# Optimization experiments

Measured on AMD Instinct MI355X. Metric: run time of the kernel, lower is better.

## Reference

```python
import jax, jax.numpy as jnp
import numpy as np

N = 50000
E = 800000
F_IN = 128
F_OUT = 128


def setup_inputs() -> dict:
    key = jax.random.key(0)
    ks = jax.random.split(key, 7)
    feature = jax.random.normal(ks[0], (N, F_IN), dtype=jnp.float32)
    self_weight = jax.random.uniform(ks[1], (N, 1), dtype=jnp.float32)
    weight = jax.random.uniform(ks[2], (E,), dtype=jnp.float32)
    src = jax.random.randint(ks[3], (E,), 0, N, dtype=jnp.int32)
    dst = jax.random.randint(ks[4], (E,), 0, N, dtype=jnp.int32)
    W = jax.random.normal(ks[5], (F_OUT, F_IN), dtype=jnp.float32) / np.sqrt(F_IN)
    b = jax.random.normal(ks[6], (F_OUT,), dtype=jnp.float32) * 0.01
    return {"feature": feature, "self_weight": self_weight, "weight": weight,
            "src": src, "dst": dst, "W": W, "b": b}


def reference(feature, self_weight, weight, src, dst, W, b):
    # messages: (w + 1) * h_src  -> [E, F_IN]
    msgs = (weight + 1.0)[:, None] * feature[src]
    # segment-sum into destination nodes -> [N, F_IN]
    agg = jax.ops.segment_sum(msgs, dst, num_segments=N)
    # self-loop affine: h * (self_weight + 1) + aggregated messages
    h = feature * (self_weight + 1.0) + agg
    # final linear: h @ W^T + b
    return h @ W.T + b
```

## Files before the change

kernel.cpp:

```cpp
#include <hip/hip_runtime.h>


#define F 128
#define NPB 32
#define CAPB 1408
#define CHUNK 4096
#define MAXNB 1600

typedef __attribute__((ext_vector_type(8))) short short8;
typedef __attribute__((ext_vector_type(4))) float f32x4;

__device__ inline unsigned short f2b(float f) {
    union { float f; unsigned u; } v; v.f = f;
    unsigned r = (v.u + 0x7fffu + ((v.u >> 16) & 1u)) >> 16;
    return (unsigned short)r;
}
__device__ inline float blo(unsigned u) { union { unsigned u; float f; } x; x.u = u << 16; return x.f; }
__device__ inline float bhi(unsigned u) { union { unsigned u; float f; } x; x.u = u & 0xffff0000u; return x.f; }

struct __align__(8) Edge { unsigned pk; float w; };

__global__ __launch_bounds__(256) void gemm_scatter(
    const float* __restrict__ feat, const float* __restrict__ W,
    const int* __restrict__ dst, const int* __restrict__ src,
    const float* __restrict__ weight,
    unsigned short* __restrict__ g, int* __restrict__ gcur,
    Edge* __restrict__ sorted, int M, int E, int GB, int NB)
{
    __shared__ __align__(16) char smem[128 * 136 * 2 + 64 * 136 * 2];
    const int tid = threadIdx.x;

    if ((int)blockIdx.x < GB) {
        unsigned short* Wl  = (unsigned short*)smem;
        unsigned short* ftl = (unsigned short*)(smem + 128 * 136 * 2);
        const int row0 = blockIdx.x * 64;

        for (int i = tid; i < 128 * 32; i += 256) {
            int r = i >> 5, c4 = i & 31;
            float4 v = ((const float4*)W)[i];
            ushort4 h; h.x = f2b(v.x); h.y = f2b(v.y); h.z = f2b(v.z); h.w = f2b(v.w);
            *(ushort4*)&Wl[r * 136 + c4 * 4] = h;
        }
        for (int i = tid; i < 64 * 32; i += 256) {
            int r = i >> 5, c4 = i & 31;
            int rr = row0 + r; if (rr >= M) rr = M - 1;
            float4 v = ((const float4*)feat)[(size_t)rr * 32 + c4];
            ushort4 h; h.x = f2b(v.x); h.y = f2b(v.y); h.z = f2b(v.z); h.w = f2b(v.w);
            *(ushort4*)&ftl[r * 136 + c4 * 4] = h;
        }
        __syncthreads();

        const int lane = tid & 63, wid = tid >> 6;
        const int m = lane & 15, quad = lane >> 4;
        const int rbase = wid * 16;

        f32x4 acc[8];
#pragma unroll
        for (int t = 0; t < 8; ++t) acc[t] = (f32x4){0.f, 0.f, 0.f, 0.f};

#pragma unroll
        for (int kk = 0; kk < 4; ++kk) {
            const int k0 = kk * 32 + quad * 8;
            short8 a = *(const short8*)&ftl[(rbase + m) * 136 + k0];
#pragma unroll
            for (int t = 0; t < 8; ++t) {
                short8 bfrag = *(const short8*)&Wl[(t * 16 + m) * 136 + k0];
                acc[t] = __builtin_amdgcn_mfma_f32_16x16x32_bf16(a, bfrag, acc[t], 0, 0, 0);
            }
        }

#pragma unroll
        for (int reg = 0; reg < 4; ++reg) {
            int r = row0 + rbase + quad * 4 + reg;
            if (r < M) {
#pragma unroll
                for (int t = 0; t < 8; ++t)
                    g[(size_t)r * F + t * 16 + m] = f2b(acc[t][reg]);
            }
        }
    } else {
        int* hist  = (int*)smem;
        int* lbase = hist + MAXNB;
        const int e0 = ((int)blockIdx.x - GB) * CHUNK;

        for (int i = tid; i < NB; i += 256) hist[i] = 0;
        __syncthreads();
#pragma unroll
        for (int j = 0; j < CHUNK / 256; ++j) {
            int e = e0 + j * 256 + tid;
            if (e < E) atomicAdd(&hist[dst[e] >> 5], 1);
        }
        __syncthreads();
        for (int i = tid; i < NB; i += 256) {
            int c = hist[i];
            lbase[i] = c ? atomicAdd(&gcur[i], c) : 0;
            hist[i] = 0;
        }
        __syncthreads();
#pragma unroll
        for (int j = 0; j < CHUNK / 256; ++j) {
            int e = e0 + j * 256 + tid;
            if (e < E) {
                int d = dst[e];
                int bkt = d >> 5;
                int pos = lbase[bkt] + atomicAdd(&hist[bkt], 1);
                if (pos < CAPB) {
                    Edge ed;
                    ed.pk = (unsigned)src[e] | ((unsigned)(d & 31) << 16);
                    ed.w = weight[e] + 1.0f;
                    sorted[(size_t)bkt * CAPB + pos] = ed;
                }
            }
        }
    }
}

__global__ __launch_bounds__(256, 6) void bucket_gather(
    const unsigned short* __restrict__ g, const Edge* __restrict__ sorted,
    const int* __restrict__ gcur, const float* __restrict__ sw,
    const float* __restrict__ bvec, float* __restrict__ out, int M)
{
    __shared__ Edge ebuf[CAPB];
    __shared__ int hcnt[NPB];
    __shared__ int off[NPB + 1];
    __shared__ int cur[NPB];

    const int b = blockIdx.x, tid = threadIdx.x;
    int cnt = gcur[b]; if (cnt > CAPB) cnt = CAPB;

    if (tid < NPB) hcnt[tid] = 0;
    __syncthreads();

    Edge held[(CAPB + 255) / 256];
    int nh = 0;
    for (int i = tid; i < cnt; i += 256) {
        Edge e = sorted[(size_t)b * CAPB + i];
        held[nh++] = e;
        atomicAdd(&hcnt[e.pk >> 16], 1);
    }
    __syncthreads();
    if (tid < NPB) {
        int v = hcnt[tid];
        int x = v;
#pragma unroll
        for (int s = 1; s < NPB; s <<= 1) {
            int t = __shfl_up(x, s, 64);
            if (tid >= s) x += t;
        }
        off[tid + 1] = x;
        if (tid == 0) off[0] = 0;
        cur[tid] = x - v;
    }
    __syncthreads();
    for (int j = 0; j < nh; ++j) {
        int dl = held[j].pk >> 16;
        int p = atomicAdd(&cur[dl], 1);
        ebuf[p] = held[j];
    }
    __syncthreads();

    const int grp = tid >> 4, c = tid & 15;
    const float4 b0 = ((const float4*)bvec)[c * 2];
    const float4 b1 = ((const float4*)bvec)[c * 2 + 1];

    for (int nn = grp; nn < NPB; nn += 16) {
        const int node = b * NPB + nn;
        if (node >= M) continue;
        int p = off[nn];
        const int pe = off[nn + 1];

        float acc[8] = {0.f, 0.f, 0.f, 0.f, 0.f, 0.f, 0.f, 0.f};
        for (; p + 1 < pe; p += 2) {
            Edge e0 = ebuf[p], e1 = ebuf[p + 1];
            const uint4 r0 = *(const uint4*)(g + (size_t)(e0.pk & 0xffffu) * F + c * 8);
            const uint4 r1 = *(const uint4*)(g + (size_t)(e1.pk & 0xffffu) * F + c * 8);
            float w0 = e0.w, w1 = e1.w;
            acc[0] = fmaf(w0, blo(r0.x), acc[0]); acc[1] = fmaf(w0, bhi(r0.x), acc[1]);
            acc[2] = fmaf(w0, blo(r0.y), acc[2]); acc[3] = fmaf(w0, bhi(r0.y), acc[3]);
            acc[4] = fmaf(w0, blo(r0.z), acc[4]); acc[5] = fmaf(w0, bhi(r0.z), acc[5]);
            acc[6] = fmaf(w0, blo(r0.w), acc[6]); acc[7] = fmaf(w0, bhi(r0.w), acc[7]);
            acc[0] = fmaf(w1, blo(r1.x), acc[0]); acc[1] = fmaf(w1, bhi(r1.x), acc[1]);
            acc[2] = fmaf(w1, blo(r1.y), acc[2]); acc[3] = fmaf(w1, bhi(r1.y), acc[3]);
            acc[4] = fmaf(w1, blo(r1.z), acc[4]); acc[5] = fmaf(w1, bhi(r1.z), acc[5]);
            acc[6] = fmaf(w1, blo(r1.w), acc[6]); acc[7] = fmaf(w1, bhi(r1.w), acc[7]);
        }
        if (p < pe) {
            Edge e0 = ebuf[p];
            const uint4 r0 = *(const uint4*)(g + (size_t)(e0.pk & 0xffffu) * F + c * 8);
            float w0 = e0.w;
            acc[0] = fmaf(w0, blo(r0.x), acc[0]); acc[1] = fmaf(w0, bhi(r0.x), acc[1]);
            acc[2] = fmaf(w0, blo(r0.y), acc[2]); acc[3] = fmaf(w0, bhi(r0.y), acc[3]);
            acc[4] = fmaf(w0, blo(r0.z), acc[4]); acc[5] = fmaf(w0, bhi(r0.z), acc[5]);
            acc[6] = fmaf(w0, blo(r0.w), acc[6]); acc[7] = fmaf(w0, bhi(r0.w), acc[7]);
        }

        const uint4 sr = *(const uint4*)(g + (size_t)node * F + c * 8);
        const float s = sw[node] + 1.0f;
        float4 o0, o1;
        o0.x = fmaf(s, blo(sr.x), b0.x) + acc[0];
        o0.y = fmaf(s, bhi(sr.x), b0.y) + acc[1];
        o0.z = fmaf(s, blo(sr.y), b0.z) + acc[2];
        o0.w = fmaf(s, bhi(sr.y), b0.w) + acc[3];
        o1.x = fmaf(s, blo(sr.z), b1.x) + acc[4];
        o1.y = fmaf(s, bhi(sr.z), b1.y) + acc[5];
        o1.z = fmaf(s, blo(sr.w), b1.z) + acc[6];
        o1.w = fmaf(s, bhi(sr.w), b1.w) + acc[7];
        float4* o = (float4*)(out + (size_t)node * F + c * 8);
        o[0] = o0; o[1] = o1;
    }
}

extern "C" void kernel_launch(void* const* d_in, const int* in_sizes, int n_in,
                              void* d_out, int out_size, void* d_ws, size_t ws_size,
                              hipStream_t stream) {
    const float* feat   = (const float*)d_in[0];
    const float* sw     = (const float*)d_in[1];
    const float* weight = (const float*)d_in[2];
    const int*   src    = (const int*)  d_in[3];
    const int*   dst    = (const int*)  d_in[4];
    const float* W      = (const float*)d_in[5];
    const float* b      = (const float*)d_in[6];
    float* out = (float*)d_out;

    const int M = in_sizes[1];
    const int E = in_sizes[2];
    const int NB = (M + NPB - 1) / NPB;
    const int GB = (M + 63) / 64;
    const int SB = (E + CHUNK - 1) / CHUNK;

    char* ws = (char*)d_ws;
    size_t og    = 0;
    size_t ocur  = ((og   + (size_t)M * F * 2) + 255) & ~(size_t)255;
    size_t osort = ((ocur + (size_t)NB * 4) + 255) & ~(size_t)255;

    unsigned short* g = (unsigned short*)(ws + og);
    int*  gcur   = (int*)(ws + ocur);
    Edge* sorted = (Edge*)(ws + osort);

    hipMemsetAsync(gcur, 0, (size_t)NB * 4, stream);
    gemm_scatter<<<GB + SB, 256, 0, stream>>>(
        feat, W, dst, src, weight, g, gcur, sorted, M, E, GB, NB);
    bucket_gather<<<NB, 256, 0, stream>>>(g, sorted, gcur, sw, b, out, M);
}
```

Measured before the change: 158.4 us.

## Split gather buckets across two blocks and read W fragments directly from global

The gather kernel now launches two blocks per 32-node bucket, each handling 16 destination nodes. Each block rescans the bucket's edge list twice from global memory instead of holding edges in registers, which doubles the parallelism and removes the per-node loop. The GEMM blocks no longer stage W into shared memory; each lane loads its W fragment from global (expected to hit cache) and converts it to bf16 inline. The aim is to cut LDS footprint and register pressure to raise occupancy, at the cost of redundant edge reads and repeated W conversions.

```diff
diff --git a/kernel.cpp b/kernel.cpp
--- a/kernel.cpp
+++ b/kernel.cpp
@@ -4,6 +4,7 @@
 #define F 128
 #define NPB 32
 #define CAPB 1408
+#define CAPH 896
 #define CHUNK 4096
 #define MAXNB 1600
 
@@ -27,20 +28,13 @@
     unsigned short* __restrict__ g, int* __restrict__ gcur,
     Edge* __restrict__ sorted, int M, int E, int GB, int NB)
 {
-    __shared__ __align__(16) char smem[128 * 136 * 2 + 64 * 136 * 2];
+    __shared__ __align__(16) char smem[64 * 136 * 2];
     const int tid = threadIdx.x;
 
     if ((int)blockIdx.x < GB) {
-        unsigned short* Wl  = (unsigned short*)smem;
-        unsigned short* ftl = (unsigned short*)(smem + 128 * 136 * 2);
+        unsigned short* ftl = (unsigned short*)smem;
         const int row0 = blockIdx.x * 64;
 
-        for (int i = tid; i < 128 * 32; i += 256) {
-            int r = i >> 5, c4 = i & 31;
-            float4 v = ((const float4*)W)[i];
-            ushort4 h; h.x = f2b(v.x); h.y = f2b(v.y); h.z = f2b(v.z); h.w = f2b(v.w);
-            *(ushort4*)&Wl[r * 136 + c4 * 4] = h;
-        }
         for (int i = tid; i < 64 * 32; i += 256) {
             int r = i >> 5, c4 = i & 31;
             int rr = row0 + r; if (rr >= M) rr = M - 1;
@@ -64,8 +58,14 @@
             short8 a = *(const short8*)&ftl[(rbase + m) * 136 + k0];
 #pragma unroll
             for (int t = 0; t < 8; ++t) {
-                short8 bfrag = *(const short8*)&Wl[(t * 16 + m) * 136 + k0];
-                acc[t] = __builtin_amdgcn_mfma_f32_16x16x32_bf16(a, bfrag, acc[t], 0, 0, 0);
+                const float4 w0 = *(const float4*)&W[(size_t)(t * 16 + m) * F + k0];
+                const float4 w1 = *(const float4*)&W[(size_t)(t * 16 + m) * F + k0 + 4];
+                short8 bf;
+                bf[0] = (short)f2b(w0.x); bf[1] = (short)f2b(w0.y);
+                bf[2] = (short)f2b(w0.z); bf[3] = (short)f2b(w0.w);
+                bf[4] = (short)f2b(w1.x); bf[5] = (short)f2b(w1.y);
+                bf[6] = (short)f2b(w1.z); bf[7] = (short)f2b(w1.w);
+                acc[t] = __builtin_amdgcn_mfma_f32_16x16x32_bf16(a, bf, acc[t], 0, 0, 0);
             }
         }
 
@@ -115,35 +115,34 @@
     }
 }
 
-__global__ __launch_bounds__(256, 6) void bucket_gather(
+__global__ __launch_bounds__(256) void bucket_gather(
     const unsigned short* __restrict__ g, const Edge* __restrict__ sorted,
     const int* __restrict__ gcur, const float* __restrict__ sw,
     const float* __restrict__ bvec, float* __restrict__ out, int M)
 {
-    __shared__ Edge ebuf[CAPB];
-    __shared__ int hcnt[NPB];
-    __shared__ int off[NPB + 1];
-    __shared__ int cur[NPB];
-
-    const int b = blockIdx.x, tid = threadIdx.x;
+    __shared__ Edge ebuf[CAPH];
+    __shared__ int hcnt[16];
+    __shared__ int off[17];
+    __shared__ int cur[16];
+
+    const int tid = threadIdx.x;
+    const int b = blockIdx.x >> 1, half = blockIdx.x & 1;
     int cnt = gcur[b]; if (cnt > CAPB) cnt = CAPB;
-
-    if (tid < NPB) hcnt[tid] = 0;
-    __syncthreads();
-
-    Edge held[(CAPB + 255) / 256];
-    int nh = 0;
+    const Edge* sb = sorted + (size_t)b * CAPB;
+
+    if (tid < 16) hcnt[tid] = 0;
+    __syncthreads();
+
     for (int i = tid; i < cnt; i += 256) {
-        Edge e = sorted[(size_t)b * CAPB + i];
-        held[nh++] = e;
-        atomicAdd(&hcnt[e.pk >> 16], 1);
-    }
-    __syncthreads();
-    if (tid < NPB) {
+        int dl = sb[i].pk >> 16;
+        if ((dl >> 4) == half) atomicAdd(&hcnt[dl & 15], 1);
+    }
+    __syncthreads();
+    if (tid < 16) {
         int v = hcnt[tid];
         int x = v;
 #pragma unroll
-        for (int s = 1; s < NPB; s <<= 1) {
+        for (int s = 1; s < 16; s <<= 1) {
             int t = __shfl_up(x, s, 64);
             if (tid >= s) x += t;
         }
@@ -152,62 +151,63 @@
         cur[tid] = x - v;
     }
     __syncthreads();
-    for (int j = 0; j < nh; ++j) {
-        int dl = held[j].pk >> 16;
-        int p = atomicAdd(&cur[dl], 1);
-        ebuf[p] = held[j];
+    for (int i = tid; i < cnt; i += 256) {
+        Edge e = sb[i];
+        int dl = e.pk >> 16;
+        if ((dl >> 4) == half) {
+            int p = atomicAdd(&cur[dl & 15], 1);
+            if (p < CAPH) ebuf[p] = e;
+        }
     }
     __syncthreads();
 
     const int grp = tid >> 4, c = tid & 15;
+    const int node = b * NPB + half * 16 + grp;
+    if (node >= M) return;
+    int p = off[grp];
+    int pe = off[grp + 1]; if (pe > CAPH) pe = CAPH;
+
     const float4 b0 = ((const float4*)bvec)[c * 2];
     const float4 b1 = ((const float4*)bvec)[c * 2 + 1];
 
-    for (int nn = grp; nn < NPB; nn += 16) {
-        const int node = b * NPB + nn;
-        if (node >= M) continue;
-        int p = off[nn];
-        const int pe = off[nn + 1];
-
-        float acc[8] = {0.f, 0.f, 0.f, 0.f, 0.f, 0.f, 0.f, 0.f};
-        for (; p + 1 < pe; p += 2) {
-            Edge e0 = ebuf[p], e1 = ebuf[p + 1];
-            const uint4 r0 = *(const uint4*)(g + (size_t)(e0.pk & 0xffffu) * F + c * 8);
-            const uint4 r1 = *(const uint4*)(g + (size_t)(e1.pk & 0xffffu) * F + c * 8);
-            float w0 = e0.w, w1 = e1.w;
-            acc[0] = fmaf(w0, blo(r0.x), acc[0]); acc[1] = fmaf(w0, bhi(r0.x), acc[1]);
-            acc[2] = fmaf(w0, blo(r0.y), acc[2]); acc[3] = fmaf(w0, bhi(r0.y), acc[3]);
-            acc[4] = fmaf(w0, blo(r0.z), acc[4]); acc[5] = fmaf(w0, bhi(r0.z), acc[5]);
-            acc[6] = fmaf(w0, blo(r0.w), acc[6]); acc[7] = fmaf(w0, bhi(r0.w), acc[7]);
-            acc[0] = fmaf(w1, blo(r1.x), acc[0]); acc[1] = fmaf(w1, bhi(r1.x), acc[1]);
-            acc[2] = fmaf(w1, blo(r1.y), acc[2]); acc[3] = fmaf(w1, bhi(r1.y), acc[3]);
-            acc[4] = fmaf(w1, blo(r1.z), acc[4]); acc[5] = fmaf(w1, bhi(r1.z), acc[5]);
-            acc[6] = fmaf(w1, blo(r1.w), acc[6]); acc[7] = fmaf(w1, bhi(r1.w), acc[7]);
-        }
-        if (p < pe) {
-            Edge e0 = ebuf[p];
-            const uint4 r0 = *(const uint4*)(g + (size_t)(e0.pk & 0xffffu) * F + c * 8);
-            float w0 = e0.w;
-            acc[0] = fmaf(w0, blo(r0.x), acc[0]); acc[1] = fmaf(w0, bhi(r0.x), acc[1]);
-            acc[2] = fmaf(w0, blo(r0.y), acc[2]); acc[3] = fmaf(w0, bhi(r0.y), acc[3]);
-            acc[4] = fmaf(w0, blo(r0.z), acc[4]); acc[5] = fmaf(w0, bhi(r0.z), acc[5]);
-            acc[6] = fmaf(w0, blo(r0.w), acc[6]); acc[7] = fmaf(w0, bhi(r0.w), acc[7]);
-        }
-
-        const uint4 sr = *(const uint4*)(g + (size_t)node * F + c * 8);
-        const float s = sw[node] + 1.0f;
-        float4 o0, o1;
-        o0.x = fmaf(s, blo(sr.x), b0.x) + acc[0];
-        o0.y = fmaf(s, bhi(sr.x), b0.y) + acc[1];
-        o0.z = fmaf(s, blo(sr.y), b0.z) + acc[2];
-        o0.w = fmaf(s, bhi(sr.y), b0.w) + acc[3];
-        o1.x = fmaf(s, blo(sr.z), b1.x) + acc[4];
-        o1.y = fmaf(s, bhi(sr.z), b1.y) + acc[5];
-        o1.z = fmaf(s, blo(sr.w), b1.z) + acc[6];
-        o1.w = fmaf(s, bhi(sr.w), b1.w) + acc[7];
-        float4* o = (float4*)(out + (size_t)node * F + c * 8);
-        o[0] = o0; o[1] = o1;
-    }
+    float acc[8] = {0.f, 0.f, 0.f, 0.f, 0.f, 0.f, 0.f, 0.f};
+    for (; p + 1 < pe; p += 2) {
+        Edge e0 = ebuf[p], e1 = ebuf[p + 1];
+        const uint4 r0 = *(const uint4*)(g + (size_t)(e0.pk & 0xffffu) * F + c * 8);
+        const uint4 r1 = *(const uint4*)(g + (size_t)(e1.pk & 0xffffu) * F + c * 8);
+        float w0 = e0.w, w1 = e1.w;
+        acc[0] = fmaf(w0, blo(r0.x), acc[0]); acc[1] = fmaf(w0, bhi(r0.x), acc[1]);
+        acc[2] = fmaf(w0, blo(r0.y), acc[2]); acc[3] = fmaf(w0, bhi(r0.y), acc[3]);
+        acc[4] = fmaf(w0, blo(r0.z), acc[4]); acc[5] = fmaf(w0, bhi(r0.z), acc[5]);
+        acc[6] = fmaf(w0, blo(r0.w), acc[6]); acc[7] = fmaf(w0, bhi(r0.w), acc[7]);
+        acc[0] = fmaf(w1, blo(r1.x), acc[0]); acc[1] = fmaf(w1, bhi(r1.x), acc[1]);
+        acc[2] = fmaf(w1, blo(r1.y), acc[2]); acc[3] = fmaf(w1, bhi(r1.y), acc[3]);
+        acc[4] = fmaf(w1, blo(r1.z), acc[4]); acc[5] = fmaf(w1, bhi(r1.z), acc[5]);
+        acc[6] = fmaf(w1, blo(r1.w), acc[6]); acc[7] = fmaf(w1, bhi(r1.w), acc[7]);
+    }
+    if (p < pe) {
+        Edge e0 = ebuf[p];
+        const uint4 r0 = *(const uint4*)(g + (size_t)(e0.pk & 0xffffu) * F + c * 8);
+        float w0 = e0.w;
+        acc[0] = fmaf(w0, blo(r0.x), acc[0]); acc[1] = fmaf(w0, bhi(r0.x), acc[1]);
+        acc[2] = fmaf(w0, blo(r0.y), acc[2]); acc[3] = fmaf(w0, bhi(r0.y), acc[3]);
+        acc[4] = fmaf(w0, blo(r0.z), acc[4]); acc[5] = fmaf(w0, bhi(r0.z), acc[5]);
+        acc[6] = fmaf(w0, blo(r0.w), acc[6]); acc[7] = fmaf(w0, bhi(r0.w), acc[7]);
+    }
+
+    const uint4 sr = *(const uint4*)(g + (size_t)node * F + c * 8);
+    const float s = sw[node] + 1.0f;
+    float4 o0, o1;
+    o0.x = fmaf(s, blo(sr.x), b0.x) + acc[0];
+    o0.y = fmaf(s, bhi(sr.x), b0.y) + acc[1];
+    o0.z = fmaf(s, blo(sr.y), b0.z) + acc[2];
+    o0.w = fmaf(s, bhi(sr.y), b0.w) + acc[3];
+    o1.x = fmaf(s, blo(sr.z), b1.x) + acc[4];
+    o1.y = fmaf(s, bhi(sr.z), b1.y) + acc[5];
+    o1.z = fmaf(s, blo(sr.w), b1.z) + acc[6];
+    o1.w = fmaf(s, bhi(sr.w), b1.w) + acc[7];
+    float4* o = (float4*)(out + (size_t)node * F + c * 8);
+    o[0] = o0; o[1] = o1;
 }
 
 extern "C" void kernel_launch(void* const* d_in, const int* in_sizes, int n_in,
@@ -240,5 +240,5 @@
     hipMemsetAsync(gcur, 0, (size_t)NB * 4, stream);
     gemm_scatter<<<GB + SB, 256, 0, stream>>>(
         feat, W, dst, src, weight, g, gcur, sorted, M, E, GB, NB);
-    bucket_gather<<<NB, 256, 0, stream>>>(g, sorted, gcur, sw, b, out, M);
-}
+    bucket_gather<<<NB * 2, 256, 0, stream>>>(g, sorted, gcur, sw, b, out, M);
+}
```

Measured after the change: 161.4 us. No clear change (+1.9%).

## Split bucket gather across column slices and load GEMM A operand directly

Applied to the files above, without the earlier changes.

Bucket size doubles to 64 nodes with larger edge chunks and capacity. The gather kernel now launches eight blocks per bucket, each covering a 16-column slice, and each block re-sorts the bucket's edges in shared memory. That trades redundant edge sorting for more parallelism and smaller per-thread loads. The GEMM path drops the shared-memory staging of feature rows and converts them to bf16 straight from global loads into MFMA fragments. Scatter blocks are moved ahead of GEMM blocks in the grid order.

```diff
diff --git a/kernel.cpp b/kernel.cpp
--- a/kernel.cpp
+++ b/kernel.cpp
@@ -2,10 +2,10 @@
 
 
 #define F 128
-#define NPB 32
-#define CAPB 1408
-#define CHUNK 4096
-#define MAXNB 1600
+#define NPB 64
+#define CAPB 2560
+#define CHUNK 16384
+#define MAXNB 800
 
 typedef __attribute__((ext_vector_type(8))) short short8;
 typedef __attribute__((ext_vector_type(4))) float f32x4;
@@ -25,34 +25,28 @@
     const int* __restrict__ dst, const int* __restrict__ src,
     const float* __restrict__ weight,
     unsigned short* __restrict__ g, int* __restrict__ gcur,
-    Edge* __restrict__ sorted, int M, int E, int GB, int NB)
+    Edge* __restrict__ sorted, int M, int E, int SB, int NB)
 {
-    __shared__ __align__(16) char smem[128 * 136 * 2 + 64 * 136 * 2];
+    __shared__ __align__(16) char smem[128 * 136 * 2];
     const int tid = threadIdx.x;
 
-    if ((int)blockIdx.x < GB) {
-        unsigned short* Wl  = (unsigned short*)smem;
-        unsigned short* ftl = (unsigned short*)(smem + 128 * 136 * 2);
-        const int row0 = blockIdx.x * 64;
-
-        for (int i = tid; i < 128 * 32; i += 256) {
+    if ((int)blockIdx.x >= SB) {
+        unsigned short* Wl = (unsigned short*)smem;
+        const int row0 = ((int)blockIdx.x - SB) * 64;
+
+        for (int i = tid; i < 4096; i += 256) {
             int r = i >> 5, c4 = i & 31;
             float4 v = ((const float4*)W)[i];
             ushort4 h; h.x = f2b(v.x); h.y = f2b(v.y); h.z = f2b(v.z); h.w = f2b(v.w);
             *(ushort4*)&Wl[r * 136 + c4 * 4] = h;
         }
-        for (int i = tid; i < 64 * 32; i += 256) {
-            int r = i >> 5, c4 = i & 31;
-            int rr = row0 + r; if (rr >= M) rr = M - 1;
-            float4 v = ((const float4*)feat)[(size_t)rr * 32 + c4];
-            ushort4 h; h.x = f2b(v.x); h.y = f2b(v.y); h.z = f2b(v.z); h.w = f2b(v.w);
-            *(ushort4*)&ftl[r * 136 + c4 * 4] = h;
-        }
         __syncthreads();
 
         const int lane = tid & 63, wid = tid >> 6;
         const int m = lane & 15, quad = lane >> 4;
         const int rbase = wid * 16;
+        int rr = row0 + rbase + m; if (rr >= M) rr = M - 1;
+        const float* frow = feat + (size_t)rr * F;
 
         f32x4 acc[8];
 #pragma unroll
@@ -61,7 +55,13 @@
 #pragma unroll
         for (int kk = 0; kk < 4; ++kk) {
             const int k0 = kk * 32 + quad * 8;
-            short8 a = *(const short8*)&ftl[(rbase + m) * 136 + k0];
+            const float4 a0 = *(const float4*)&frow[k0];
+            const float4 a1 = *(const float4*)&frow[k0 + 4];
+            short8 a;
+            a[0] = (short)f2b(a0.x); a[1] = (short)f2b(a0.y);
+            a[2] = (short)f2b(a0.z); a[3] = (short)f2b(a0.w);
+            a[4] = (short)f2b(a1.x); a[5] = (short)f2b(a1.y);
+            a[6] = (short)f2b(a1.z); a[7] = (short)f2b(a1.w);
 #pragma unroll
             for (int t = 0; t < 8; ++t) {
                 short8 bfrag = *(const short8*)&Wl[(t * 16 + m) * 136 + k0];
@@ -81,14 +81,13 @@
     } else {
         int* hist  = (int*)smem;
         int* lbase = hist + MAXNB;
-        const int e0 = ((int)blockIdx.x - GB) * CHUNK;
+        const int e0 = (int)blockIdx.x * CHUNK;
 
         for (int i = tid; i < NB; i += 256) hist[i] = 0;
         __syncthreads();
-#pragma unroll
         for (int j = 0; j < CHUNK / 256; ++j) {
             int e = e0 + j * 256 + tid;
-            if (e < E) atomicAdd(&hist[dst[e] >> 5], 1);
+            if (e < E) atomicAdd(&hist[dst[e] >> 6], 1);
         }
         __syncthreads();
         for (int i = tid; i < NB; i += 256) {
@@ -97,16 +96,15 @@
             hist[i] = 0;
         }
         __syncthreads();
-#pragma unroll
         for (int j = 0; j < CHUNK / 256; ++j) {
             int e = e0 + j * 256 + tid;
             if (e < E) {
                 int d = dst[e];
-                int bkt = d >> 5;
+                int bkt = d >> 6;
                 int pos = lbase[bkt] + atomicAdd(&hist[bkt], 1);
                 if (pos < CAPB) {
                     Edge ed;
-                    ed.pk = (unsigned)src[e] | ((unsigned)(d & 31) << 16);
+                    ed.pk = (unsigned)src[e] | ((unsigned)(d & 63) << 16);
                     ed.w = weight[e] + 1.0f;
                     sorted[(size_t)bkt * CAPB + pos] = ed;
                 }
@@ -115,7 +113,7 @@
     }
 }
 
-__global__ __launch_bounds__(256, 6) void bucket_gather(
+__global__ __launch_bounds__(256) void bucket_gather(
     const unsigned short* __restrict__ g, const Edge* __restrict__ sorted,
     const int* __restrict__ gcur, const float* __restrict__ sw,
     const float* __restrict__ bvec, float* __restrict__ out, int M)
@@ -125,89 +123,72 @@
     __shared__ int off[NPB + 1];
     __shared__ int cur[NPB];
 
-    const int b = blockIdx.x, tid = threadIdx.x;
+    const int tid = threadIdx.x;
+    const int s = (int)blockIdx.x & 7;
+    const int b = (int)blockIdx.x >> 3;
     int cnt = gcur[b]; if (cnt > CAPB) cnt = CAPB;
+    const Edge* sb = sorted + (size_t)b * CAPB;
 
     if (tid < NPB) hcnt[tid] = 0;
     __syncthreads();
-
-    Edge held[(CAPB + 255) / 256];
-    int nh = 0;
-    for (int i = tid; i < cnt; i += 256) {
-        Edge e = sorted[(size_t)b * CAPB + i];
-        held[nh++] = e;
-        atomicAdd(&hcnt[e.pk >> 16], 1);
-    }
+    for (int i = tid; i < cnt; i += 256)
+        atomicAdd(&hcnt[sb[i].pk >> 16], 1);
     __syncthreads();
     if (tid < NPB) {
         int v = hcnt[tid];
         int x = v;
 #pragma unroll
-        for (int s = 1; s < NPB; s <<= 1) {
-            int t = __shfl_up(x, s, 64);
-            if (tid >= s) x += t;
+        for (int st = 1; st < NPB; st <<= 1) {
+            int t = __shfl_up(x, st, 64);
+            if (tid >= st) x += t;
         }
         off[tid + 1] = x;
         if (tid == 0) off[0] = 0;
         cur[tid] = x - v;
     }
     __syncthreads();
-    for (int j = 0; j < nh; ++j) {
-        int dl = held[j].pk >> 16;
-        int p = atomicAdd(&cur[dl], 1);
-        ebuf[p] = held[j];
-    }
-    __syncthreads();
-
-    const int grp = tid >> 4, c = tid & 15;
-    const float4 b0 = ((const float4*)bvec)[c * 2];
-    const float4 b1 = ((const float4*)bvec)[c * 2 + 1];
-
-    for (int nn = grp; nn < NPB; nn += 16) {
-        const int node = b * NPB + nn;
-        if (node >= M) continue;
-        int p = off[nn];
-        const int pe = off[nn + 1];
-
-        float acc[8] = {0.f, 0.f, 0.f, 0.f, 0.f, 0.f, 0.f, 0.f};
-        for (; p + 1 < pe; p += 2) {
-            Edge e0 = ebuf[p], e1 = ebuf[p + 1];
-            const uint4 r0 = *(const uint4*)(g + (size_t)(e0.pk & 0xffffu) * F + c * 8);
-            const uint4 r1 = *(const uint4*)(g + (size_t)(e1.pk & 0xffffu) * F + c * 8);
-            float w0 = e0.w, w1 = e1.w;
-            acc[0] = fmaf(w0, blo(r0.x), acc[0]); acc[1] = fmaf(w0, bhi(r0.x), acc[1]);
-            acc[2] = fmaf(w0, blo(r0.y), acc[2]); acc[3] = fmaf(w0, bhi(r0.y), acc[3]);
-            acc[4] = fmaf(w0, blo(r0.z), acc[4]); acc[5] = fmaf(w0, bhi(r0.z), acc[5]);
-            acc[6] = fmaf(w0, blo(r0.w), acc[6]); acc[7] = fmaf(w0, bhi(r0.w), acc[7]);
-            acc[0] = fmaf(w1, blo(r1.x), acc[0]); acc[1] = fmaf(w1, bhi(r1.x), acc[1]);
-            acc[2] = fmaf(w1, blo(r1.y), acc[2]); acc[3] = fmaf(w1, bhi(r1.y), acc[3]);
-            acc[4] = fmaf(w1, blo(r1.z), acc[4]); acc[5] = fmaf(w1, bhi(r1.z), acc[5]);
-            acc[6] = fmaf(w1, blo(r1.w), acc[6]); acc[7] = fmaf(w1, bhi(r1.w), acc[7]);
-        }
-        if (p < pe) {
-            Edge e0 = ebuf[p];
-            const uint4 r0 = *(const uint4*)(g + (size_t)(e0.pk & 0xffffu) * F + c * 8);
-            float w0 = e0.w;
-            acc[0] = fmaf(w0, blo(r0.x), acc[0]); acc[1] = fmaf(w0, bhi(r0.x), acc[1]);
-            acc[2] = fmaf(w0, blo(r0.y), acc[2]); acc[3] = fmaf(w0, bhi(r0.y), acc[3]);
-            acc[4] = fmaf(w0, blo(r0.z), acc[4]); acc[5] = fmaf(w0, bhi(r0.z), acc[5]);
-            acc[6] = fmaf(w0, blo(r0.w), acc[6]); acc[7] = fmaf(w0, bhi(r0.w), acc[7]);
-        }
-
-        const uint4 sr = *(const uint4*)(g + (size_t)node * F + c * 8);
-        const float s = sw[node] + 1.0f;
-        float4 o0, o1;
-        o0.x = fmaf(s, blo(sr.x), b0.x) + acc[0];
-        o0.y = fmaf(s, bhi(sr.x), b0.y) + acc[1];
-        o0.z = fmaf(s, blo(sr.y), b0.z) + acc[2];
-        o0.w = fmaf(s, bhi(sr.y), b0.w) + acc[3];
-        o1.x = fmaf(s, blo(sr.z), b1.x) + acc[4];
-        o1.y = fmaf(s, bhi(sr.z), b1.y) + acc[5];
-        o1.z = fmaf(s, blo(sr.w), b1.z) + acc[6];
-        o1.w = fmaf(s, bhi(sr.w), b1.w) + acc[7];
-        float4* o = (float4*)(out + (size_t)node * F + c * 8);
-        o[0] = o0; o[1] = o1;
-    }
+    for (int i = tid; i < cnt; i += 256) {
+        Edge e = sb[i];
+        int p = atomicAdd(&cur[e.pk >> 16], 1);
+        ebuf[p] = e;
+    }
+    __syncthreads();
+
+    const int grp = tid >> 2, l = tid & 3;
+    const int node = b * NPB + grp;
+    if (node >= M) return;
+    const int cb = s * 16 + l * 4;
+    int p = off[grp];
+    const int pe = off[grp + 1];
+
+    float acc[4] = {0.f, 0.f, 0.f, 0.f};
+    for (; p + 1 < pe; p += 2) {
+        Edge e0 = ebuf[p], e1 = ebuf[p + 1];
+        const uint2 r0 = *(const uint2*)(g + (size_t)(e0.pk & 0xffffu) * F + cb);
+        const uint2 r1 = *(const uint2*)(g + (size_t)(e1.pk & 0xffffu) * F + cb);
+        float w0 = e0.w, w1 = e1.w;
+        acc[0] = fmaf(w0, blo(r0.x), acc[0]); acc[1] = fmaf(w0, bhi(r0.x), acc[1]);
+        acc[2] = fmaf(w0, blo(r0.y), acc[2]); acc[3] = fmaf(w0, bhi(r0.y), acc[3]);
+        acc[0] = fmaf(w1, blo(r1.x), acc[0]); acc[1] = fmaf(w1, bhi(r1.x), acc[1]);
+        acc[2] = fmaf(w1, blo(r1.y), acc[2]); acc[3] = fmaf(w1, bhi(r1.y), acc[3]);
+    }
+    if (p < pe) {
+        Edge e0 = ebuf[p];
+        const uint2 r0 = *(const uint2*)(g + (size_t)(e0.pk & 0xffffu) * F + cb);
+        float w0 = e0.w;
+        acc[0] = fmaf(w0, blo(r0.x), acc[0]); acc[1] = fmaf(w0, bhi(r0.x), acc[1]);
+        acc[2] = fmaf(w0, blo(r0.y), acc[2]); acc[3] = fmaf(w0, bhi(r0.y), acc[3]);
+    }
+
+    const uint2 sr = *(const uint2*)(g + (size_t)node * F + cb);
+    const float4 bb = *(const float4*)&bvec[cb];
+    const float sc = sw[node] + 1.0f;
+    float4 o;
+    o.x = fmaf(sc, blo(sr.x), bb.x) + acc[0];
+    o.y = fmaf(sc, bhi(sr.x), bb.y) + acc[1];
+    o.z = fmaf(sc, blo(sr.y), bb.z) + acc[2];
+    o.w = fmaf(sc, bhi(sr.y), bb.w) + acc[3];
+    *(float4*)(out + (size_t)node * F + cb) = o;
 }
 
 extern "C" void kernel_launch(void* const* d_in, const int* in_sizes, int n_in,
@@ -238,7 +219,7 @@
     Edge* sorted = (Edge*)(ws + osort);
 
     hipMemsetAsync(gcur, 0, (size_t)NB * 4, stream);
-    gemm_scatter<<<GB + SB, 256, 0, stream>>>(
-        feat, W, dst, src, weight, g, gcur, sorted, M, E, GB, NB);
-    bucket_gather<<<NB, 256, 0, stream>>>(g, sorted, gcur, sw, b, out, M);
-}
+    gemm_scatter<<<SB + GB, 256, 0, stream>>>(
+        feat, W, dst, src, weight, g, gcur, sorted, M, E, SB, NB);
+    bucket_gather<<<NB * 8, 256, 0, stream>>>(g, sorted, gcur, sw, b, out, M);
+}
```

After: 218.9 us. +38.2%, slower.

## Pre-convert features and W to bf16 in init kernel, reorder scatter blocks first

Applied to the files above, without the earlier changes.

Adds an init kernel that converts features and W to bf16 in global memory and zeroes the bucket counters, which replaces the memset. The GEMM blocks then load bf16 A fragments straight from global memory and copy W without converting it. Scatter blocks are now placed before the GEMM blocks. The gather kernel re-reads edges from global memory instead of holding them in registers, drops the occupancy hint, and shrinks bucket capacity to 1024 with extra bounds clamps. The cost is an extra pass writing and reading a bf16 copy of the features, one more kernel launch, and a risk of dropping edges if any bucket exceeds 1024.

```diff
diff --git a/kernel.cpp b/kernel.cpp
--- a/kernel.cpp
+++ b/kernel.cpp
@@ -3,7 +3,7 @@
 
 #define F 128
 #define NPB 32
-#define CAPB 1408
+#define CAPB 1024
 #define CHUNK 4096
 #define MAXNB 1600
 
@@ -20,39 +20,56 @@
 
 struct __align__(8) Edge { unsigned pk; float w; };
 
+__global__ __launch_bounds__(256) void init_kernel(
+    const float* __restrict__ feat, const float* __restrict__ W,
+    unsigned short* __restrict__ featbf, unsigned short* __restrict__ wbf,
+    int* __restrict__ gcur, int n4f, int n4w, int nb)
+{
+    int i = blockIdx.x * 256 + threadIdx.x;
+    if (i < n4f) {
+        float4 v = ((const float4*)feat)[i];
+        ushort4 h; h.x = f2b(v.x); h.y = f2b(v.y); h.z = f2b(v.z); h.w = f2b(v.w);
+        ((ushort4*)featbf)[i] = h;
+    } else if (i < n4f + n4w) {
+        int j = i - n4f;
+        float4 v = ((const float4*)W)[j];
+        ushort4 h; h.x = f2b(v.x); h.y = f2b(v.y); h.z = f2b(v.z); h.w = f2b(v.w);
+        ((ushort4*)wbf)[j] = h;
+    } else if (i - n4f - n4w < nb) {
+        gcur[i - n4f - n4w] = 0;
+    }
+}
+
 __global__ __launch_bounds__(256) void gemm_scatter(
-    const float* __restrict__ feat, const float* __restrict__ W,
+    const unsigned short* __restrict__ featbf, const unsigned short* __restrict__ wbf,
     const int* __restrict__ dst, const int* __restrict__ src,
     const float* __restrict__ weight,
     unsigned short* __restrict__ g, int* __restrict__ gcur,
-    Edge* __restrict__ sorted, int M, int E, int GB, int NB)
+    Edge* __restrict__ sorted, int M, int E, int SB, int NB)
 {
-    __shared__ __align__(16) char smem[128 * 136 * 2 + 64 * 136 * 2];
+    __shared__ __align__(16) char smem[128 * 136 * 2];
     const int tid = threadIdx.x;
 
-    if ((int)blockIdx.x < GB) {
-        unsigned short* Wl  = (unsigned short*)smem;
-        unsigned short* ftl = (unsigned short*)(smem + 128 * 136 * 2);
-        const int row0 = blockIdx.x * 64;
-
-        for (int i = tid; i < 128 * 32; i += 256) {
-            int r = i >> 5, c4 = i & 31;
-            float4 v = ((const float4*)W)[i];
-            ushort4 h; h.x = f2b(v.x); h.y = f2b(v.y); h.z = f2b(v.z); h.w = f2b(v.w);
-            *(ushort4*)&Wl[r * 136 + c4 * 4] = h;
-        }
-        for (int i = tid; i < 64 * 32; i += 256) {
-            int r = i >> 5, c4 = i & 31;
-            int rr = row0 + r; if (rr >= M) rr = M - 1;
-            float4 v = ((const float4*)feat)[(size_t)rr * 32 + c4];
-            ushort4 h; h.x = f2b(v.x); h.y = f2b(v.y); h.z = f2b(v.z); h.w = f2b(v.w);
-            *(ushort4*)&ftl[r * 136 + c4 * 4] = h;
+    if ((int)blockIdx.x >= SB) {
+        unsigned short* Wl = (unsigned short*)smem;
+        const int row0 = ((int)blockIdx.x - SB) * 64;
+
+        for (int i = tid; i < 2048; i += 256) {
+            int r = i >> 4, c8 = i & 15;
+            *(uint4*)&Wl[r * 136 + c8 * 8] = *(const uint4*)&wbf[r * 128 + c8 * 8];
         }
         __syncthreads();
 
         const int lane = tid & 63, wid = tid >> 6;
         const int m = lane & 15, quad = lane >> 4;
         const int rbase = wid * 16;
+        int rr = row0 + rbase + m; if (rr >= M) rr = M - 1;
+        const unsigned short* frow = featbf + (size_t)rr * F;
+
+        short8 afrag[4];
+#pragma unroll
+        for (int kk = 0; kk < 4; ++kk)
+            afrag[kk] = *(const short8*)&frow[kk * 32 + quad * 8];
 
         f32x4 acc[8];
 #pragma unroll
@@ -61,11 +78,10 @@
 #pragma unroll
         for (int kk = 0; kk < 4; ++kk) {
             const int k0 = kk * 32 + quad * 8;
-            short8 a = *(const short8*)&ftl[(rbase + m) * 136 + k0];
 #pragma unroll
             for (int t = 0; t < 8; ++t) {
                 short8 bfrag = *(const short8*)&Wl[(t * 16 + m) * 136 + k0];
-                acc[t] = __builtin_amdgcn_mfma_f32_16x16x32_bf16(a, bfrag, acc[t], 0, 0, 0);
+                acc[t] = __builtin_amdgcn_mfma_f32_16x16x32_bf16(afrag[kk], bfrag, acc[t], 0, 0, 0);
             }
         }
 
@@ -81,7 +97,7 @@
     } else {
         int* hist  = (int*)smem;
         int* lbase = hist + MAXNB;
-        const int e0 = ((int)blockIdx.x - GB) * CHUNK;
+        const int e0 = (int)blockIdx.x * CHUNK;
 
         for (int i = tid; i < NB; i += 256) hist[i] = 0;
         __syncthreads();
@@ -115,7 +131,7 @@
     }
 }
 
-__global__ __launch_bounds__(256, 6) void bucket_gather(
+__global__ __launch_bounds__(256) void bucket_gather(
     const unsigned short* __restrict__ g, const Edge* __restrict__ sorted,
     const int* __restrict__ gcur, const float* __restrict__ sw,
     const float* __restrict__ bvec, float* __restrict__ out, int M)
@@ -127,17 +143,12 @@
 
     const int b = blockIdx.x, tid = threadIdx.x;
     int cnt = gcur[b]; if (cnt > CAPB) cnt = CAPB;
+    const Edge* sb = sorted + (size_t)b * CAPB;
 
     if (tid < NPB) hcnt[tid] = 0;
     __syncthreads();
-
-    Edge held[(CAPB + 255) / 256];
-    int nh = 0;
-    for (int i = tid; i < cnt; i += 256) {
-        Edge e = sorted[(size_t)b * CAPB + i];
-        held[nh++] = e;
-        atomicAdd(&hcnt[e.pk >> 16], 1);
-    }
+    for (int i = tid; i < cnt; i += 256)
+        atomicAdd(&hcnt[sb[i].pk >> 16], 1);
     __syncthreads();
     if (tid < NPB) {
         int v = hcnt[tid];
@@ -152,10 +163,10 @@
         cur[tid] = x - v;
     }
     __syncthreads();
-    for (int j = 0; j < nh; ++j) {
-        int dl = held[j].pk >> 16;
-        int p = atomicAdd(&cur[dl], 1);
-        ebuf[p] = held[j];
+    for (int i = tid; i < cnt; i += 256) {
+        Edge e = sb[i];
+        int p = atomicAdd(&cur[e.pk >> 16], 1);
+        if (p < CAPB) ebuf[p] = e;
     }
     __syncthreads();
 
@@ -167,7 +178,7 @@
         const int node = b * NPB + nn;
         if (node >= M) continue;
         int p = off[nn];
-        const int pe = off[nn + 1];
+        int pe = off[nn + 1]; if (pe > CAPB) pe = CAPB;
 
         float acc[8] = {0.f, 0.f, 0.f, 0.f, 0.f, 0.f, 0.f, 0.f};
         for (; p + 1 < pe; p += 2) {
@@ -230,15 +241,22 @@
 
     char* ws = (char*)d_ws;
     size_t og    = 0;
-    size_t ocur  = ((og   + (size_t)M * F * 2) + 255) & ~(size_t)255;
+    size_t ofbf  = ((og   + (size_t)M * F * 2) + 255) & ~(size_t)255;
+    size_t owbf  = ((ofbf + (size_t)M * F * 2) + 255) & ~(size_t)255;
+    size_t ocur  = ((owbf + (size_t)F * F * 2) + 255) & ~(size_t)255;
     size_t osort = ((ocur + (size_t)NB * 4) + 255) & ~(size_t)255;
 
-    unsigned short* g = (unsigned short*)(ws + og);
+    unsigned short* g      = (unsigned short*)(ws + og);
+    unsigned short* featbf = (unsigned short*)(ws + ofbf);
+    unsigned short* wbf    = (unsigned short*)(ws + owbf);
     int*  gcur   = (int*)(ws + ocur);
     Edge* sorted = (Edge*)(ws + osort);
 
-    hipMemsetAsync(gcur, 0, (size_t)NB * 4, stream);
-    gemm_scatter<<<GB + SB, 256, 0, stream>>>(
-        feat, W, dst, src, weight, g, gcur, sorted, M, E, GB, NB);
+    const int n4f = M * F / 4, n4w = F * F / 4;
+    const int initN = n4f + n4w + NB;
+    init_kernel<<<(initN + 255) / 256, 256, 0, stream>>>(
+        feat, W, featbf, wbf, gcur, n4f, n4w, NB);
+    gemm_scatter<<<SB + GB, 256, 0, stream>>>(
+        featbf, wbf, dst, src, weight, g, gcur, sorted, M, E, SB, NB);
     bucket_gather<<<NB, 256, 0, stream>>>(g, sorted, gcur, sw, b, out, M);
 }
```

Result: faster. 146.8 us (-7.3%).
